# Optimization experiments

Measured on AMD Instinct MI355X. Metric: run time of the kernel, lower is better.

The kernel has to match this reference:

```python
import jax, jax.numpy as jnp
import numpy as np

NUM_HEADS = 16
HEAD_DIM = 128
D_MODEL = 2048
BATCH = 2
SEQ = 2048


def setup_inputs() -> dict:
    key = jax.random.key(0)
    ks = jax.random.split(key, 6)
    x = jax.random.normal(ks[0], (BATCH, SEQ, D_MODEL), dtype=jnp.float32)
    # RoPE tables (real/imag parts of freqs_cis), shape [S, HEAD_DIM//2]
    pos = jnp.arange(SEQ, dtype=jnp.float32)[:, None]
    inv_freq = 1.0 / (10000.0 ** (jnp.arange(0, HEAD_DIM, 2, dtype=jnp.float32) / HEAD_DIM))
    ang = pos * inv_freq[None, :]
    freq_cos = jnp.cos(ang)
    freq_sin = jnp.sin(ang)
    scale = 1.0 / np.sqrt(D_MODEL)
    wq = jax.random.normal(ks[1], (D_MODEL, NUM_HEADS * HEAD_DIM), dtype=jnp.float32) * scale
    wk = jax.random.normal(ks[2], (D_MODEL, NUM_HEADS * HEAD_DIM), dtype=jnp.float32) * scale
    wv = jax.random.normal(ks[3], (D_MODEL, NUM_HEADS * HEAD_DIM), dtype=jnp.float32) * scale
    wo = jax.random.normal(ks[4], (NUM_HEADS * HEAD_DIM, D_MODEL), dtype=jnp.float32) * scale
    return {"x": x, "freq_cos": freq_cos, "freq_sin": freq_sin,
            "wq": wq, "wk": wk, "wv": wv, "wo": wo}


def _rotate_half(t):
    half = t.shape[-1] // 2
    return jnp.concatenate([-t[..., half:], t[..., :half]], axis=-1)


def _apply_rope(q, k, freq_cos, freq_sin):
    # q, k: [B, H, S, D]; freq_cos/sin: [S_total, D//2]
    q = q.astype(jnp.float32)
    k = k.astype(jnp.float32)
    S = q.shape[2]
    cos = jnp.concatenate([freq_cos[:S], freq_cos[:S]], axis=-1)[None, None]  # [1,1,S,D]
    sin = jnp.concatenate([freq_sin[:S], freq_sin[:S]], axis=-1)[None, None]
    q_out = q * cos + _rotate_half(q) * sin
    k_out = k * cos + _rotate_half(k) * sin
    return q_out, k_out


def reference(x, freq_cos, freq_sin, wq, wk, wv, wo):
    B, S, D = x.shape
    H, hd = NUM_HEADS, HEAD_DIM
    q = (x @ wq).reshape(B, S, H, hd).transpose(0, 2, 1, 3)  # [B,H,S,hd]
    k = (x @ wk).reshape(B, S, H, hd).transpose(0, 2, 1, 3)
    v = (x @ wv).reshape(B, S, H, hd).transpose(0, 2, 1, 3)
    q, k = _apply_rope(q, k, freq_cos, freq_sin)
    # explicit causal attention (faithful to CPU/GPU path)
    logits = jnp.einsum('bhqd,bhkd->bhqk', q, k) / jnp.sqrt(jnp.float32(hd))
    mask = jnp.tril(jnp.ones((S, S), dtype=jnp.float32))
    logits = jnp.where(mask[None, None, :, :], logits, -1e10)
    weights = jax.nn.softmax(logits, axis=-1)
    out = jnp.einsum('bhqk,bhkd->bhqd', weights, v)  # [B,H,S,hd]
    out = out.transpose(0, 2, 1, 3).reshape(B, S, H * hd)
    return out @ wo
```

## Files before the change

kernel.cpp:

```cpp
#include <hip/hip_runtime.h>

typedef unsigned short u16;
typedef unsigned int u32;
typedef __attribute__((ext_vector_type(8))) short bf16x8;
typedef __attribute__((ext_vector_type(4))) short bf16x4;
typedef __attribute__((ext_vector_type(4))) float f32x4;
typedef __attribute__((ext_vector_type(16))) float f32x16;

#define MFMA(a, b, c) __builtin_amdgcn_mfma_f32_16x16x32_bf16(a, b, c, 0, 0, 0)
#define MFMA32(a, b, c) __builtin_amdgcn_mfma_f32_32x32x16_bf16(a, b, c, 0, 0, 0)
#define ASYNC16(g, l)                                                        \
  __builtin_amdgcn_global_load_lds(                                          \
      (const __attribute__((address_space(1))) u32*)(g),                     \
      (__attribute__((address_space(3))) u32*)(l), 16, 0, 0)

__device__ __forceinline__ float b2f(u16 u) {
  union { u32 i; float f; } x; x.i = ((u32)u) << 16; return x.f;
}
__device__ __forceinline__ u16 f2b(float f) {
  union { float f; u32 i; } x; x.f = f;
  return (u16)((x.i + 0x7fff + ((x.i >> 16) & 1)) >> 16);
}
__device__ __forceinline__ f32x4 fzero4() { f32x4 z = {0.f, 0.f, 0.f, 0.f}; return z; }
__device__ __forceinline__ f32x16 fzero16() {
  f32x16 z;
#pragma unroll
  for (int i = 0; i < 16; ++i) z[i] = 0.f;
  return z;
}
__device__ __forceinline__ u32 pkbf16(float lo, float hi) {
  u32 r;
  asm("v_cvt_pk_bf16_f32 %0, %1, %2" : "=v"(r) : "v"(lo), "v"(hi));
  return r;
}

__global__ __launch_bounds__(256) void cvt_x(const float* __restrict__ src,
                                             u16* __restrict__ dst) {
  const int i = (blockIdx.x * 256 + threadIdx.x) * 4;
  const f32x4 v = *(const f32x4*)(src + i);
  bf16x4 o;
  o[0] = (short)f2b(v[0]); o[1] = (short)f2b(v[1]);
  o[2] = (short)f2b(v[2]); o[3] = (short)f2b(v[3]);
  *(bf16x4*)(dst + i) = o;
}

__global__ __launch_bounds__(256) void wtrans_f32(const float* __restrict__ src,
                                                  u16* __restrict__ dst) {
  __shared__ u16 tile[64][65];
  const int k0 = blockIdx.y * 64, n0 = blockIdx.x * 64;
  const int t = threadIdx.x;
  const int tr = t >> 3, tc = t & 7;

#pragma unroll
  for (int hh = 0; hh < 2; ++hh) {
    const int k = tr + hh * 32;
    const float* p = src + (size_t)(k0 + k) * 2048 + n0 + tc * 8;
    const f32x4 a = *(const f32x4*)(p);
    const f32x4 b = *(const f32x4*)(p + 4);
#pragma unroll
    for (int j = 0; j < 4; ++j) tile[k][tc * 8 + j] = f2b(a[j]);
#pragma unroll
    for (int j = 0; j < 4; ++j) tile[k][tc * 8 + 4 + j] = f2b(b[j]);
  }
  __syncthreads();
#pragma unroll
  for (int hh = 0; hh < 2; ++hh) {
    const int n = tr + hh * 32;
    bf16x8 v;
#pragma unroll
    for (int j = 0; j < 8; ++j) v[j] = (short)tile[tc * 8 + j][n];
    *(bf16x8*)(dst + (size_t)(n0 + n) * 2048 + k0 + tc * 8) = v;
  }
}

__global__ __launch_bounds__(256) void wtrans3(const float* __restrict__ wq,
                                               const float* __restrict__ wk,
                                               const float* __restrict__ wv,
                                               u16* __restrict__ wTall) {
  __shared__ u16 tile[64][65];
  const int z = blockIdx.z;
  const float* src = (z == 0) ? wq : (z == 1) ? wk : wv;
  u16* dst = wTall + (size_t)z * 2048 * 2048;
  const int k0 = blockIdx.y * 64, n0 = blockIdx.x * 64;
  const int t = threadIdx.x;
  const int tr = t >> 3, tc = t & 7;

#pragma unroll
  for (int hh = 0; hh < 2; ++hh) {
    const int k = tr + hh * 32;
    const float* p = src + (size_t)(k0 + k) * 2048 + n0 + tc * 8;
    const f32x4 a = *(const f32x4*)(p);
    const f32x4 b = *(const f32x4*)(p + 4);
#pragma unroll
    for (int j = 0; j < 4; ++j) tile[k][tc * 8 + j] = f2b(a[j]);
#pragma unroll
    for (int j = 0; j < 4; ++j) tile[k][tc * 8 + 4 + j] = f2b(b[j]);
  }
  __syncthreads();
#pragma unroll
  for (int hh = 0; hh < 2; ++hh) {
    const int n = tr + hh * 32;
    bf16x8 v;
#pragma unroll
    for (int j = 0; j < 8; ++j) v[j] = (short)tile[tc * 8 + j][n];
    *(bf16x8*)(dst + (size_t)(n0 + n) * 2048 + k0 + tc * 8) = v;
  }
}

__device__ __forceinline__ void gemm_mainloop(const u16* __restrict__ A,
                                              const u16* __restrict__ Bt,
                                              int K, int m0, int n0,
                                              u16* lA, u16* lB,
                                              f32x4 acc[4][4]) {
  const int tid = threadIdx.x;
  const int lane = tid & 63;
  const int wave = tid >> 6;
  const int quad = lane >> 4;
  const int l16 = lane & 15;
  const int wr = wave >> 1, wc = wave & 1;

  const int srow = lane >> 2;
  const int scol = (lane & 3) * 8;
  const u16* ga0 = A + (size_t)(m0 + (wave * 2 + 0) * 16 + srow) * K + scol;
  const u16* ga1 = A + (size_t)(m0 + (wave * 2 + 1) * 16 + srow) * K + scol;
  const u16* gb0 = Bt + (size_t)(n0 + (wave * 2 + 0) * 16 + srow) * K + scol;
  const u16* gb1 = Bt + (size_t)(n0 + (wave * 2 + 1) * 16 + srow) * K + scol;
  u16* la0 = lA + (wave * 2 + 0) * 512;
  u16* la1 = lA + (wave * 2 + 1) * 512;
  u16* lb0 = lB + (wave * 2 + 0) * 512;
  u16* lb1 = lB + (wave * 2 + 1) * 512;

  for (int k0 = 0; k0 < K; k0 += 32) {
    ASYNC16(ga0 + k0, la0);
    ASYNC16(ga1 + k0, la1);
    ASYNC16(gb0 + k0, lb0);
    ASYNC16(gb1 + k0, lb1);
    __syncthreads();
    bf16x8 af[4], bfr[4];
#pragma unroll
    for (int mb = 0; mb < 4; ++mb)
      af[mb] = *(const bf16x8*)(lA + ((wr * 64 + mb * 16 + l16) * 32 + quad * 8));
#pragma unroll
    for (int nb = 0; nb < 4; ++nb)
      bfr[nb] = *(const bf16x8*)(lB + ((wc * 64 + nb * 16 + l16) * 32 + quad * 8));
#pragma unroll
    for (int mb = 0; mb < 4; ++mb)
#pragma unroll
      for (int nb = 0; nb < 4; ++nb)
        acc[mb][nb] = MFMA(af[mb], bfr[nb], acc[mb][nb]);
    __syncthreads();
  }
}

__global__ __launch_bounds__(256) void gemm_qkv(const u16* __restrict__ x,
                                                const u16* __restrict__ wT,
                                                u16* __restrict__ qkv) {
  __shared__ u16 lA[128 * 32];
  __shared__ u16 lB[128 * 32];
  f32x4 acc[4][4];
#pragma unroll
  for (int i = 0; i < 4; ++i)
#pragma unroll
    for (int j = 0; j < 4; ++j) acc[i][j] = fzero4();

  const int m0 = blockIdx.y * 128, n0 = blockIdx.x * 128;
  gemm_mainloop(x, wT, 2048, m0, n0, lA, lB, acc);

  const int lane = threadIdx.x & 63, wave = threadIdx.x >> 6;
  const int quad = lane >> 4, l16 = lane & 15;
  const int wr = wave >> 1, wc = wave & 1;
#pragma unroll
  for (int mb = 0; mb < 4; ++mb)
#pragma unroll
    for (int nb = 0; nb < 4; ++nb)
#pragma unroll
      for (int r = 0; r < 4; ++r) {
        const int row = m0 + wr * 64 + mb * 16 + quad * 4 + r;
        const int col = n0 + wc * 64 + nb * 16 + l16;
        const int b = row >> 11, s = row & 2047;
        const int which = col >> 11, rem = col & 2047;
        const int hh = rem >> 7, d = rem & 127;
        const size_t idx = (size_t)which * ((size_t)4096 * 2048) +
                           (((size_t)(b * 16 + hh) * 2048 + s) * 128 + d);
        qkv[idx] = f2b(acc[mb][nb][r]);
      }
}

__global__ __launch_bounds__(256) void gemm_out(const u16* __restrict__ Oin,
                                                const u16* __restrict__ woT,
                                                float* __restrict__ out) {
  __shared__ u16 lA[128 * 32];
  __shared__ u16 lB[128 * 32];
  f32x4 acc[4][4];
#pragma unroll
  for (int i = 0; i < 4; ++i)
#pragma unroll
    for (int j = 0; j < 4; ++j) acc[i][j] = fzero4();

  const int m0 = blockIdx.y * 128, n0 = blockIdx.x * 128;
  gemm_mainloop(Oin, woT, 2048, m0, n0, lA, lB, acc);

  const int lane = threadIdx.x & 63, wave = threadIdx.x >> 6;
  const int quad = lane >> 4, l16 = lane & 15;
  const int wr = wave >> 1, wc = wave & 1;
#pragma unroll
  for (int mb = 0; mb < 4; ++mb)
#pragma unroll
    for (int nb = 0; nb < 4; ++nb)
#pragma unroll
      for (int r = 0; r < 4; ++r) {
        const int row = m0 + wr * 64 + mb * 16 + quad * 4 + r;
        const int col = n0 + wc * 64 + nb * 16 + l16;
        out[(size_t)row * 2048 + col] = acc[mb][nb][r];
      }
}

__global__ __launch_bounds__(256) void rope_kernel(u16* __restrict__ Q,
                                                   u16* __restrict__ K,
                                                   const float* __restrict__ fcos,
                                                   const float* __restrict__ fsin) {
  const int i = blockIdx.x * 256 + threadIdx.x;
  const int d = i & 63;
  const int s = (i >> 6) & 2047;
  const int bh = i >> 17;
  const size_t base = ((size_t)bh * 2048 + s) * 128;
  const float c = fcos[s * 64 + d];
  const float sn = fsin[s * 64 + d];
  const float qs = 0.08838834764831845f;

  const float q0 = b2f(Q[base + d]), q1 = b2f(Q[base + d + 64]);
  Q[base + d] = f2b((q0 * c - q1 * sn) * qs);
  Q[base + d + 64] = f2b((q1 * c + q0 * sn) * qs);
  const float k0 = b2f(K[base + d]), k1 = b2f(K[base + d + 64]);
  K[base + d] = f2b(k0 * c - k1 * sn);
  K[base + d + 64] = f2b(k1 * c + k0 * sn);
}

template <int NB>
__device__ __forceinline__ void qkt_block(f32x16& sv, int n0, int qlo, int hi,
                                          int c, const u16* lK,
                                          const bf16x8* qf) {
  const int lo = n0 + NB * 32;
  if (lo < qlo + 32) {
    sv = fzero16();
#pragma unroll
    for (int kc = 0; kc < 8; ++kc) {
      const bf16x8 kf =
          *(const bf16x8*)(lK + (NB * 32 + c) * 136 + kc * 16 + hi * 8);
      sv = MFMA32(kf, qf[kc], sv);
    }
    if (lo == qlo) {
#pragma unroll
      for (int r = 0; r < 16; ++r) {
        const int n32 = (r & 3) + 8 * (r >> 2) + 4 * hi;
        if (n32 > c) sv[r] = -1e30f;
      }
    }
  } else {
#pragma unroll
    for (int r = 0; r < 16; ++r) sv[r] = -1e30f;
  }
}

template <int NB>
__device__ __forceinline__ void pv_block(const f32x16& sv, int n0, int qlo,
                                         int hi, int c, const u16* lV,
                                         f32x16* accO) {
  if (n0 + NB * 32 < qlo + 32) {
#pragma unroll
    for (int half = 0; half < 2; ++half) {
      const int rb = half * 8;
      const u32 pA = pkbf16(sv[rb + 0], sv[rb + 1]);
      const u32 pB = pkbf16(sv[rb + 2], sv[rb + 3]);
      const u32 pC = pkbf16(sv[rb + 4], sv[rb + 5]);
      const u32 pD = pkbf16(sv[rb + 6], sv[rb + 7]);
      const u32 xA = (u32)__shfl_xor((int)pA, 32);
      const u32 xB = (u32)__shfl_xor((int)pB, 32);
      const u32 xC = (u32)__shfl_xor((int)pC, 32);
      const u32 xD = (u32)__shfl_xor((int)pD, 32);
      bf16x8 pa;
      u32* pw = (u32*)&pa;
      pw[0] = hi ? xC : pA;
      pw[1] = hi ? xD : pB;
      pw[2] = hi ? pC : xA;
      pw[3] = hi ? pD : xB;
#pragma unroll
      for (int db = 0; db < 4; ++db) {
        const bf16x8 vf = *(const bf16x8*)(lV + (db * 32 + c) * 72 +
                                           NB * 32 + half * 16 + hi * 8);
        accO[db] = MFMA32(pa, vf, accO[db]);
      }
    }
  }
}

__global__ __launch_bounds__(256, 2) void attn4(const u16* __restrict__ Q,
                                                const u16* __restrict__ K,
                                                const u16* __restrict__ V,
                                                u16* __restrict__ O) {
  __shared__ u16 lK[64 * 136];
  __shared__ u16 lV[128 * 72];

  const int bid = blockIdx.x;
  const int bh = (bid & 7) + 8 * ((bid >> 3) & 3);
  const int tq = bid >> 5;
  const int qt = (tq < 8) ? tq : 23 - tq;
  const int q0 = qt * 128;
  const int b = bh >> 4, h = bh & 15;
  const u16* Qh = Q + (size_t)bh * 2048 * 128;
  const u16* Kh = K + (size_t)bh * 2048 * 128;
  const u16* Vh = V + (size_t)bh * 2048 * 128;

  const int tid = threadIdx.x;
  const int lane = tid & 63, wave = tid >> 6;
  const int hi = lane >> 5, c = lane & 31;
  const int qlo = q0 + wave * 32;
  const int krow = tid >> 4, kj = tid & 15;
  const int r0 = (tid & 31) * 2, d0v = (tid >> 5) * 16;

  bf16x8 qf[8];
  {
    const u16* qrow = Qh + (size_t)(q0 + wave * 32 + c) * 128 + hi * 8;
#pragma unroll
    for (int kc = 0; kc < 8; ++kc) qf[kc] = *(const bf16x8*)(qrow + kc * 16);
  }

  float m_i = -1e30f, l_i = 0.f;
  f32x16 accO[4];
#pragma unroll
  for (int db = 0; db < 4; ++db) accO[db] = fzero16();

  const int nIter = 2 * qt + 2;

  bf16x8 kreg[4], vreg[4];
  {
#pragma unroll
    for (int i = 0; i < 4; ++i)
      kreg[i] = *(const bf16x8*)(Kh + (size_t)(krow + 16 * i) * 128 + kj * 8);
    const u16* vp = Vh + (size_t)r0 * 128 + d0v;
    vreg[0] = *(const bf16x8*)(vp);
    vreg[1] = *(const bf16x8*)(vp + 8);
    vreg[2] = *(const bf16x8*)(vp + 128);
    vreg[3] = *(const bf16x8*)(vp + 136);
  }

  for (int it = 0; it < nIter; ++it) {
    const int n0 = it * 64;
#pragma unroll
    for (int i = 0; i < 4; ++i)
      *(bf16x8*)(lK + (krow + 16 * i) * 136 + kj * 8) = kreg[i];
#pragma unroll
    for (int j = 0; j < 8; ++j) {
      const u32 lo = (u16)vreg[0][j], hi2 = (u16)vreg[2][j];
      *(u32*)(lV + (d0v + j) * 72 + r0) = lo | (hi2 << 16);
    }
#pragma unroll
    for (int j = 0; j < 8; ++j) {
      const u32 lo = (u16)vreg[1][j], hi2 = (u16)vreg[3][j];
      *(u32*)(lV + (d0v + 8 + j) * 72 + r0) = lo | (hi2 << 16);
    }
    __syncthreads();

    if (it + 1 < nIter) {
      const int nn = n0 + 64;
#pragma unroll
      for (int i = 0; i < 4; ++i)
        kreg[i] =
            *(const bf16x8*)(Kh + (size_t)(nn + krow + 16 * i) * 128 + kj * 8);
      const u16* vp = Vh + (size_t)(nn + r0) * 128 + d0v;
      vreg[0] = *(const bf16x8*)(vp);
      vreg[1] = *(const bf16x8*)(vp + 8);
      vreg[2] = *(const bf16x8*)(vp + 128);
      vreg[3] = *(const bf16x8*)(vp + 136);
    }

    f32x16 s0, s1;
    qkt_block<0>(s0, n0, qlo, hi, c, lK, qf);
    qkt_block<1>(s1, n0, qlo, hi, c, lK, qf);

    float mx = -1e30f;
#pragma unroll
    for (int r = 0; r < 16; ++r) mx = fmaxf(mx, fmaxf(s0[r], s1[r]));
    mx = fmaxf(mx, __shfl_xor(mx, 32));
    const float mn = fmaxf(m_i, mx);
    const float alpha = __expf(m_i - mn);
    m_i = mn;
    float rs = 0.f;
#pragma unroll
    for (int r = 0; r < 16; ++r) {
      const float p0 = __expf(s0[r] - mn);
      const float p1 = __expf(s1[r] - mn);
      s0[r] = p0; s1[r] = p1;
      rs += p0 + p1;
    }
    rs += __shfl_xor(rs, 32);
    l_i = l_i * alpha + rs;

#pragma unroll
    for (int r = 0; r < 16; ++r) {
      const int src = ((r & 3) + 8 * (r >> 2) + 4 * hi) + (lane & 32);
      const float aa = __shfl(alpha, src);
      accO[0][r] *= aa; accO[1][r] *= aa;
      accO[2][r] *= aa; accO[3][r] *= aa;
    }

    pv_block<0>(s0, n0, qlo, hi, c, lV, accO);
    pv_block<1>(s1, n0, qlo, hi, c, lV, accO);
    __syncthreads();
  }

  const float linv = 1.f / l_i;
#pragma unroll
  for (int r = 0; r < 16; ++r) {
    const int q32 = (r & 3) + 8 * (r >> 2) + 4 * hi;
    const float inv = __shfl(linv, q32 + (lane & 32));
    const int srow = q0 + wave * 32 + q32;
    u16* orow = O + ((size_t)b * 2048 + srow) * 2048 + h * 128 + c;
#pragma unroll
    for (int db = 0; db < 4; ++db) orow[db * 32] = f2b(accO[db][r] * inv);
  }
}

extern "C" void kernel_launch(void* const* d_in, const int* in_sizes, int n_in,
                              void* d_out, int out_size, void* d_ws, size_t ws_size,
                              hipStream_t stream) {
  const float* x  = (const float*)d_in[0];
  const float* fc = (const float*)d_in[1];
  const float* fs = (const float*)d_in[2];
  const float* wq = (const float*)d_in[3];
  const float* wk = (const float*)d_in[4];
  const float* wv = (const float*)d_in[5];
  const float* wo = (const float*)d_in[6];
  float* out = (float*)d_out;

  u16* ws = (u16*)d_ws;
  const size_t BUF = (size_t)4096 * 2048;
  u16* xb  = ws;
  u16* Ob  = ws;
  u16* Qb  = ws + 1 * BUF;
  u16* Kb  = ws + 2 * BUF;
  u16* Vb  = ws + 3 * BUF;
  u16* wTall = (u16*)d_out;
  u16* woT = Kb;

  hipLaunchKernelGGL(cvt_x, dim3(8192), dim3(256), 0, stream, x, xb);
  hipLaunchKernelGGL(wtrans3, dim3(32, 32, 3), dim3(256), 0, stream, wq, wk, wv, wTall);
  hipLaunchKernelGGL(gemm_qkv, dim3(48, 32), dim3(256), 0, stream, xb, wTall, Qb);
  hipLaunchKernelGGL(rope_kernel, dim3(16384), dim3(256), 0, stream, Qb, Kb, fc, fs);
  hipLaunchKernelGGL(attn4, dim3(512), dim3(256), 0, stream, Qb, Kb, Vb, Ob);
  hipLaunchKernelGGL(wtrans_f32, dim3(32, 32), dim3(256), 0, stream, wo, woT);
  hipLaunchKernelGGL(gemm_out, dim3(16, 32), dim3(256), 0, stream, Ob, woT, out);
}
```

Measured before the change: 393.5 us.

## Rewrite output GEMM as 256x128 triple-buffered kernel, add lazy softmax rescale

Replaces the output projection GEMM with a 512-thread, 256x128-tile kernel that uses triple-buffered async global-to-LDS loads, XOR-swizzled LDS layout, a remapped block order and split-phase barriers. This is meant to improve data reuse and overlap load latency with compute. In attention, MFMA sections are wrapped in s_setprio, and the online-softmax rescale of the accumulator is skipped unless the running max grows by more than 8. The skip removes shuffles and multiplies but lets exp values reach up to e^8 before bf16 packing.

Measured after the change: 388.9 us. Within noise of the previous version (-1.2%).

```diff
diff --git a/kernel.cpp b/kernel.cpp
--- a/kernel.cpp
+++ b/kernel.cpp
@@ -13,6 +13,13 @@
   __builtin_amdgcn_global_load_lds(                                          \
       (const __attribute__((address_space(1))) u32*)(g),                     \
       (__attribute__((address_space(3))) u32*)(l), 16, 0, 0)
+
+#define SBARRIER()                                                           \
+  do {                                                                       \
+    asm volatile("" ::: "memory");                                           \
+    __builtin_amdgcn_s_barrier();                                            \
+    asm volatile("" ::: "memory");                                           \
+  } while (0)
 
 __device__ __forceinline__ float b2f(u16 u) {
   union { u32 i; float f; } x; x.i = ((u32)u) << 16; return x.f;
@@ -186,31 +193,124 @@
       }
 }
 
-__global__ __launch_bounds__(256) void gemm_out(const u16* __restrict__ Oin,
-                                                const u16* __restrict__ woT,
-                                                float* __restrict__ out) {
-  __shared__ u16 lA[128 * 32];
-  __shared__ u16 lB[128 * 32];
-  f32x4 acc[4][4];
-#pragma unroll
-  for (int i = 0; i < 4; ++i)
-#pragma unroll
-    for (int j = 0; j < 4; ++j) acc[i][j] = fzero4();
-
-  const int m0 = blockIdx.y * 128, n0 = blockIdx.x * 128;
-  gemm_mainloop(Oin, woT, 2048, m0, n0, lA, lB, acc);
-
-  const int lane = threadIdx.x & 63, wave = threadIdx.x >> 6;
+__global__ __launch_bounds__(512, 2) void gemm_out8(const u16* __restrict__ Oin,
+                                                    const u16* __restrict__ woT,
+                                                    float* __restrict__ out) {
+  __shared__ u16 lds[3 * 24576];
+
+  const int orig = blockIdx.x;
+  const int wg = (orig & 7) * 32 + (orig >> 3);
+  const int m0 = (wg >> 4) * 256;
+  const int n0 = (wg & 15) * 128;
+
+  const int tid = threadIdx.x;
+  const int lane = tid & 63;
+  const int wave = tid >> 6;
   const int quad = lane >> 4, l16 = lane & 15;
-  const int wr = wave >> 1, wc = wave & 1;
-#pragma unroll
-  for (int mb = 0; mb < 4; ++mb)
-#pragma unroll
-    for (int nb = 0; nb < 4; ++nb)
+  const int wr = wave >> 2, wc = wave & 3;
+
+  const int r0s = tid >> 3;
+  const int c0s = (tid & 7) ^ (r0s & 7);
+  const int r1s = r0s + 64;
+  const int c1s = (tid & 7) ^ (r1s & 7);
+
+  const u16* gA = Oin + (size_t)m0 * 2048;
+  const u16* gB = woT + (size_t)n0 * 2048;
+
+#define SLOT8(t) (lds + ((t) % 3) * 24576)
+#define STAGE_A8(t)                                                          \
+  do {                                                                       \
+    u16* Lb0 = SLOT8(t) + wave * 512;                                        \
+    const u16* g0 = gA + (t) * 64;                                           \
+    ASYNC16(g0 + (size_t)r0s * 2048 + c0s * 8, Lb0);                         \
+    ASYNC16(g0 + (size_t)r1s * 2048 + c1s * 8, Lb0 + 4096);                  \
+    u16* Lb1 = SLOT8(t) + 8192 + wave * 512;                                 \
+    const u16* g1 = gA + (size_t)128 * 2048 + (t) * 64;                      \
+    ASYNC16(g1 + (size_t)r0s * 2048 + c0s * 8, Lb1);                         \
+    ASYNC16(g1 + (size_t)r1s * 2048 + c1s * 8, Lb1 + 4096);                  \
+  } while (0)
+#define STAGE_B8(t)                                                          \
+  do {                                                                       \
+    u16* Lb = SLOT8(t) + 16384 + wave * 512;                                 \
+    const u16* g = gB + (t) * 64;                                            \
+    ASYNC16(g + (size_t)r0s * 2048 + c0s * 8, Lb);                           \
+    ASYNC16(g + (size_t)r1s * 2048 + c1s * 8, Lb + 4096);                    \
+  } while (0)
+
+  f32x4 acc[8][2];
+#pragma unroll
+  for (int i = 0; i < 8; ++i) { acc[i][0] = fzero4(); acc[i][1] = fzero4(); }
+
+  int aoff[8], boff[2];
+#pragma unroll
+  for (int mb = 0; mb < 8; ++mb) aoff[mb] = (wr * 128 + mb * 16 + l16) * 64;
+#pragma unroll
+  for (int nb = 0; nb < 2; ++nb) boff[nb] = 16384 + (wc * 32 + nb * 16 + l16) * 64;
+  const int ach0 = ((0 * 4 + quad) ^ (l16 & 7)) * 8;
+  const int ach1 = ((1 * 4 + quad) ^ (l16 & 7)) * 8;
+
+  STAGE_A8(0); STAGE_B8(0);
+  STAGE_A8(1); STAGE_B8(1);
+  asm volatile("s_waitcnt vmcnt(6)" ::: "memory");
+  SBARRIER();
+
+  for (int t = 0; t < 32; ++t) {
+    const u16* sl = SLOT8(t);
+    bf16x8 af[8], bfr[2];
+
+#pragma unroll
+    for (int mb = 0; mb < 8; ++mb)
+      af[mb] = *(const bf16x8*)(sl + aoff[mb] + ach0);
+#pragma unroll
+    for (int nb = 0; nb < 2; ++nb)
+      bfr[nb] = *(const bf16x8*)(sl + boff[nb] + ach0);
+    if (t < 30) STAGE_A8(t + 2);
+    SBARRIER();
+    asm volatile("s_waitcnt lgkmcnt(0)" ::: "memory");
+    __builtin_amdgcn_s_setprio(1);
+#pragma unroll
+    for (int mb = 0; mb < 8; ++mb)
+#pragma unroll
+      for (int nb = 0; nb < 2; ++nb)
+        acc[mb][nb] = MFMA(af[mb], bfr[nb], acc[mb][nb]);
+    __builtin_amdgcn_s_setprio(0);
+    SBARRIER();
+
+#pragma unroll
+    for (int mb = 0; mb < 8; ++mb)
+      af[mb] = *(const bf16x8*)(sl + aoff[mb] + ach1);
+#pragma unroll
+    for (int nb = 0; nb < 2; ++nb)
+      bfr[nb] = *(const bf16x8*)(sl + boff[nb] + ach1);
+    if (t < 30) STAGE_B8(t + 2);
+    SBARRIER();
+    asm volatile("s_waitcnt lgkmcnt(0)" ::: "memory");
+    __builtin_amdgcn_s_setprio(1);
+#pragma unroll
+    for (int mb = 0; mb < 8; ++mb)
+#pragma unroll
+      for (int nb = 0; nb < 2; ++nb)
+        acc[mb][nb] = MFMA(af[mb], bfr[nb], acc[mb][nb]);
+    __builtin_amdgcn_s_setprio(0);
+    if (t <= 29) {
+      asm volatile("s_waitcnt vmcnt(6)" ::: "memory");
+    } else if (t == 30) {
+      asm volatile("s_waitcnt vmcnt(0)" ::: "memory");
+    }
+    SBARRIER();
+  }
+#undef SLOT8
+#undef STAGE_A8
+#undef STAGE_B8
+
+#pragma unroll
+  for (int mb = 0; mb < 8; ++mb)
+#pragma unroll
+    for (int nb = 0; nb < 2; ++nb)
 #pragma unroll
       for (int r = 0; r < 4; ++r) {
-        const int row = m0 + wr * 64 + mb * 16 + quad * 4 + r;
-        const int col = n0 + wc * 64 + nb * 16 + l16;
+        const int row = m0 + wr * 128 + mb * 16 + quad * 4 + r;
+        const int col = n0 + wc * 32 + nb * 16 + l16;
         out[(size_t)row * 2048 + col] = acc[mb][nb][r];
       }
 }
@@ -243,12 +343,14 @@
   const int lo = n0 + NB * 32;
   if (lo < qlo + 32) {
     sv = fzero16();
+    __builtin_amdgcn_s_setprio(1);
 #pragma unroll
     for (int kc = 0; kc < 8; ++kc) {
       const bf16x8 kf =
           *(const bf16x8*)(lK + (NB * 32 + c) * 136 + kc * 16 + hi * 8);
       sv = MFMA32(kf, qf[kc], sv);
     }
+    __builtin_amdgcn_s_setprio(0);
     if (lo == qlo) {
 #pragma unroll
       for (int r = 0; r < 16; ++r) {
@@ -284,12 +386,14 @@
       pw[1] = hi ? xD : pB;
       pw[2] = hi ? pC : xA;
       pw[3] = hi ? pD : xB;
+      __builtin_amdgcn_s_setprio(1);
 #pragma unroll
       for (int db = 0; db < 4; ++db) {
         const bf16x8 vf = *(const bf16x8*)(lV + (db * 32 + c) * 72 +
                                            NB * 32 + half * 16 + hi * 8);
         accO[db] = MFMA32(pa, vf, accO[db]);
       }
+      __builtin_amdgcn_s_setprio(0);
     }
   }
 }
@@ -382,27 +486,29 @@
 #pragma unroll
     for (int r = 0; r < 16; ++r) mx = fmaxf(mx, fmaxf(s0[r], s1[r]));
     mx = fmaxf(mx, __shfl_xor(mx, 32));
-    const float mn = fmaxf(m_i, mx);
-    const float alpha = __expf(m_i - mn);
-    m_i = mn;
+    if (!__all(mx - m_i <= 8.0f)) {
+      const float mn = fmaxf(m_i, mx);
+      const float alpha = __expf(m_i - mn);
+      m_i = mn;
+      l_i *= alpha;
+#pragma unroll
+      for (int r = 0; r < 16; ++r) {
+        const int src = ((r & 3) + 8 * (r >> 2) + 4 * hi) + (lane & 32);
+        const float aa = __shfl(alpha, src);
+        accO[0][r] *= aa; accO[1][r] *= aa;
+        accO[2][r] *= aa; accO[3][r] *= aa;
+      }
+    }
     float rs = 0.f;
 #pragma unroll
     for (int r = 0; r < 16; ++r) {
-      const float p0 = __expf(s0[r] - mn);
-      const float p1 = __expf(s1[r] - mn);
+      const float p0 = __expf(s0[r] - m_i);
+      const float p1 = __expf(s1[r] - m_i);
       s0[r] = p0; s1[r] = p1;
       rs += p0 + p1;
     }
     rs += __shfl_xor(rs, 32);
-    l_i = l_i * alpha + rs;
-
-#pragma unroll
-    for (int r = 0; r < 16; ++r) {
-      const int src = ((r & 3) + 8 * (r >> 2) + 4 * hi) + (lane & 32);
-      const float aa = __shfl(alpha, src);
-      accO[0][r] *= aa; accO[1][r] *= aa;
-      accO[2][r] *= aa; accO[3][r] *= aa;
-    }
+    l_i += rs;
 
     pv_block<0>(s0, n0, qlo, hi, c, lV, accO);
     pv_block<1>(s1, n0, qlo, hi, c, lV, accO);
@@ -449,5 +555,5 @@
   hipLaunchKernelGGL(rope_kernel, dim3(16384), dim3(256), 0, stream, Qb, Kb, fc, fs);
   hipLaunchKernelGGL(attn4, dim3(512), dim3(256), 0, stream, Qb, Kb, Vb, Ob);
   hipLaunchKernelGGL(wtrans_f32, dim3(32, 32), dim3(256), 0, stream, wo, woT);
-  hipLaunchKernelGGL(gemm_out, dim3(16, 32), dim3(256), 0, stream, Ob, woT, out);
-}
+  hipLaunchKernelGGL(gemm_out8, dim3(256), dim3(512), 0, stream, Ob, woT, out);
+}
```
